# Optimization experiments

Hardware: AMD Instinct MI355X
Metric: run time of the kernel (lower is better)

The kernel has to match this reference:

```python
import jax, jax.numpy as jnp
import numpy as np

B, NA, NB = 2, 2048, 2048
DIM_A, DIM_B = 256, 256
HEADS, DH_A, DH_B = 8, 64, 64
INNER_A, INNER_B = DH_A * HEADS, DH_B * HEADS
EPS = 1e-5


def layer_norm(x, w, b):
    m = jnp.mean(x, axis=-1, keepdims=True)
    v = jnp.mean(jnp.square(x - m), axis=-1, keepdims=True)
    return (x - m) * jax.lax.rsqrt(v + EPS) * w + b


def setup_inputs() -> dict:
    key = jax.random.key(0)
    ks = jax.random.split(key, 16)
    s = 0.02
    return {
        "feat_a": jax.random.normal(ks[0], (B, NA, DIM_A), jnp.float32),
        "feat_b": jax.random.normal(ks[1], (B, NB, DIM_B), jnp.float32),
        "mask_a_b": jax.random.bernoulli(ks[2], 0.5, (B, NA, NB)),
        # linear weights stored (in, out)
        "Wq": jax.random.normal(ks[3], (DIM_A, INNER_B), jnp.float32) * s,
        "bq": jnp.zeros((INNER_B,), jnp.float32),
        "Wk": jax.random.normal(ks[4], (DIM_B, INNER_B), jnp.float32) * s,
        "bk": jnp.zeros((INNER_B,), jnp.float32),
        "Wv": jax.random.normal(ks[5], (DIM_B, INNER_A), jnp.float32) * s,
        "bv": jnp.zeros((INNER_A,), jnp.float32),
        "Wg": jax.random.normal(ks[6], (DIM_A, INNER_A), jnp.float32) * s,
        "bg": jnp.zeros((INNER_A,), jnp.float32),
        "Wo": jax.random.normal(ks[7], (INNER_A, DIM_A), jnp.float32) * s,
        "bo": jnp.zeros((DIM_A,), jnp.float32),
        "ln_a_w": jnp.ones((DIM_A,), jnp.float32),
        "ln_a_b": jnp.zeros((DIM_A,), jnp.float32),
        "ln_b_w": jnp.ones((DIM_B,), jnp.float32),
        "ln_b_b": jnp.zeros((DIM_B,), jnp.float32),
        "qln_w": jnp.ones((INNER_B,), jnp.float32),
        "qln_b": jnp.zeros((INNER_B,), jnp.float32),
        "kln_w": jnp.ones((INNER_B,), jnp.float32),
        "kln_b": jnp.zeros((INNER_B,), jnp.float32),
    }


def reference(feat_a, feat_b, mask_a_b, Wq, bq, Wk, bk, Wv, bv, Wg, bg, Wo, bo,
              ln_a_w, ln_a_b, ln_b_w, ln_b_b, qln_w, qln_b, kln_w, kln_b):
    scale = DH_B ** -0.5
    fa = layer_norm(feat_a, ln_a_w, ln_a_b)            # (b, na, dim_a)
    fb = layer_norm(feat_b, ln_b_w, ln_b_b)            # (b, nb, dim_b)
    q = layer_norm(fa @ Wq + bq, qln_w, qln_b)         # (b, na, inner_b)
    k = layer_norm(fb @ Wk + bk, kln_w, kln_b)         # (b, nb, inner_b)
    v = fb @ Wv + bv                                   # (b, nb, inner_a)
    g = fa @ Wg + bg                                   # (b, na, inner_a)
    q = q.reshape(B, NA, HEADS, DH_B)
    k = k.reshape(B, NB, HEADS, DH_B)
    v = v.reshape(B, NB, HEADS, DH_A)
    g = g.reshape(B, NA, HEADS, DH_A)
    sim = jnp.einsum('bihd,bjhd->bhij', q, k) * scale  # (b, h, na, nb)
    neg = jnp.finfo(sim.dtype).min
    sim = jnp.where(mask_a_b[:, None, :, :], sim, neg)
    attn = jax.nn.softmax(sim, axis=-1)
    out = jnp.einsum('bhij,bjhd->bihd', attn, v)       # (b, na, h, dh_a)
    out = jax.nn.sigmoid(g) * out
    out = out.reshape(B, NA, INNER_A)
    return out @ Wo + bo                               # (b, na, dim_a)
```

## Files before the change

### kernel.cpp

```cpp
#include <hip/hip_runtime.h>
#include <hip/hip_bf16.h>

using bf16 = __hip_bfloat16;
typedef short bf16x8 __attribute__((ext_vector_type(8)));
typedef float f32x4 __attribute__((ext_vector_type(4)));
typedef float f32x16 __attribute__((ext_vector_type(16)));
typedef unsigned short ushort8_t __attribute__((ext_vector_type(8)));
typedef unsigned long long u64;

static constexpr int NA_ = 2048, NB_ = 2048;
static constexpr int H_ = 8, DH_ = 64, INNER_ = 512;
static constexpr int MROWS = 2 * NA_;

#define MFMA32(a, b, c) __builtin_amdgcn_mfma_f32_16x16x32_bf16(a, b, c, 0, 0, 0)
#define MFMA3216(a, b, c) __builtin_amdgcn_mfma_f32_32x32x16_bf16(a, b, c, 0, 0, 0)

__device__ __forceinline__ unsigned short bfbits(float x) {
  bf16 h = __float2bfloat16(x);
  return __builtin_bit_cast(unsigned short, h);
}
__device__ __forceinline__ float b2f(unsigned short u) {
  unsigned v = ((unsigned)u) << 16;
  return __builtin_bit_cast(float, v);
}

__global__ __launch_bounds__(256) void prep_kernel(
    const float* __restrict__ fa_in, const float* __restrict__ fb_in,
    const float* __restrict__ law, const float* __restrict__ lab,
    const float* __restrict__ lbw, const float* __restrict__ lbb,
    bf16* __restrict__ fa, bf16* __restrict__ fb,
    const float* __restrict__ Wq, const float* __restrict__ Wk,
    const float* __restrict__ Wv, const float* __restrict__ Wg,
    const float* __restrict__ Wo,
    bf16* __restrict__ Wqt, bf16* __restrict__ Wkt,
    bf16* __restrict__ Wvt, bf16* __restrict__ Wgt,
    bf16* __restrict__ Woth, bf16* __restrict__ Wotl,
    const void* __restrict__ maskp, u64* __restrict__ mbits) {
  int blk = blockIdx.x;
  int t = threadIdx.x;
  if (blk < 2048) {
    int row = blk * 4 + (t >> 6);
    int lane = t & 63;
    const float *src, *w, *bb;
    bf16* dst;
    int r;
    if (row < MROWS) { src = fa_in; w = law; bb = lab; dst = fa; r = row; }
    else             { src = fb_in; w = lbw; bb = lbb; dst = fb; r = row - MROWS; }
    float4 x = *(const float4*)(src + (size_t)r * 256 + lane * 4);
    float s  = (x.x + x.y) + (x.z + x.w);
    float s2 = (x.x * x.x + x.y * x.y) + (x.z * x.z + x.w * x.w);
#pragma unroll
    for (int m = 32; m >= 1; m >>= 1) { s += __shfl_xor(s, m); s2 += __shfl_xor(s2, m); }
    float mean = s * (1.0f / 256.0f);
    float var  = s2 * (1.0f / 256.0f) - mean * mean;
    float rstd = rsqrtf(var + 1e-5f);
    float4 wv = *(const float4*)(w + lane * 4);
    float4 bv = *(const float4*)(bb + lane * 4);
    ushort4 o;
    o.x = bfbits((x.x - mean) * rstd * wv.x + bv.x);
    o.y = bfbits((x.y - mean) * rstd * wv.y + bv.y);
    o.z = bfbits((x.z - mean) * rstd * wv.z + bv.z);
    o.w = bfbits((x.w - mean) * rstd * wv.w + bv.w);
    *(ushort4*)(dst + (size_t)r * 256 + lane * 4) = o;
  } else if (blk < 4608) {
    int z = (blk - 2048) >> 9;
    int idx = ((blk - 2048) & 511) * 256 + t;
    if (z < 4) {
      const float* W = (z == 0) ? Wq : (z == 1) ? Wk : (z == 2) ? Wv : Wg;
      bf16* Wt = (z == 0) ? Wqt : (z == 1) ? Wkt : (z == 2) ? Wvt : Wgt;
      int kk = idx >> 9, n = idx & 511;
      Wt[n * 256 + kk] = __float2bfloat16(W[idx]);
    } else {
      int kk = idx >> 8, n = idx & 255;
      float w = Wo[idx];
      bf16 hi = __float2bfloat16(w);
      Woth[n * 512 + kk] = hi;
      Wotl[n * 512 + kk] = __float2bfloat16(w - __bfloat162float(hi));
    }
  } else {
    __shared__ unsigned shf[4];
    const unsigned char* mu = (const unsigned char*)maskp;
    bool nz = ((t & 3) != 0) && (mu[t] != 0);
    u64 bal = __ballot(nz);
    if ((t & 63) == 0) shf[t >> 6] = (bal != 0ull) ? 1u : 0u;
    __syncthreads();
    bool m8 = (shf[0] | shf[1] | shf[2] | shf[3]) != 0;
    int lane = t & 63, wid = t >> 6;
    int lb = blk - 4608;
    for (size_t word = (size_t)lb * 4 + wid; word < 131072; word += 8192) {
      size_t e = word * 64 + lane;
      int v = m8 ? (int)mu[e] : ((const int*)maskp)[e];
      u64 b2 = __ballot(v != 0);
      if (lane == 0) mbits[word] = b2;
    }
  }
}

__global__ __launch_bounds__(256) void gemm4_kernel(
    const bf16* __restrict__ fa, const bf16* __restrict__ fb,
    const bf16* __restrict__ Wqt, const bf16* __restrict__ Wkt,
    const bf16* __restrict__ Wgt, const bf16* __restrict__ Wvt,
    const float* __restrict__ bq, const float* __restrict__ bk,
    const float* __restrict__ bg, const float* __restrict__ bv,
    const float* __restrict__ qlw, const float* __restrict__ qlb,
    const float* __restrict__ klw, const float* __restrict__ klb,
    bf16* __restrict__ qo, bf16* __restrict__ ko,
    bf16* __restrict__ gout, bf16* __restrict__ vout) {
  __shared__ __align__(16) char sm[27648];
  int z = blockIdx.z;
  int t = threadIdx.x, wave = t >> 6, lane = t & 63;
  int lm = lane & 15, quad = lane >> 4, q8 = quad * 8;

  if (z < 2) {
    bf16* As = (bf16*)sm;
    float* Pred = (float*)(sm + 16896);
    float* MV   = (float*)(sm + 17408);
    const bf16* A    = z ? fb : fa;
    const bf16* Wt   = z ? Wkt : Wqt;
    const float* bias = z ? bk : bq;
    const float* lw  = z ? klw : qlw;
    const float* lb  = z ? klb : qlb;
    bf16* out        = z ? ko : qo;
    int m0 = blockIdx.x * 16;
#pragma unroll
    for (int i = 0; i < 2; i++) {
      int id = t + 256 * i, r = id >> 5, cg = id & 31;
      *(ushort8_t*)(&As[r * 264 + cg * 8]) =
          *(const ushort8_t*)(A + (size_t)(m0 + r) * 256 + cg * 8);
    }
    __syncthreads();
    int n0w = wave * 128;
    f32x4 acc[8] = {};
    const bf16* wrow[8];
#pragma unroll
    for (int ni = 0; ni < 8; ni++) wrow[ni] = Wt + (size_t)(n0w + ni * 16 + lm) * 256;
#pragma unroll
    for (int ks = 0; ks < 8; ks++) {
      int k0 = ks * 32;
      bf16x8 af = *(const bf16x8*)(&As[lm * 264 + k0 + q8]);
#pragma unroll
      for (int ni = 0; ni < 8; ni++) {
        bf16x8 bf_ = *(const bf16x8*)(wrow[ni] + k0 + q8);
        acc[ni] = MFMA32(af, bf_, acc[ni]);
      }
    }
    float bvv[8];
#pragma unroll
    for (int ni = 0; ni < 8; ni++) bvv[ni] = bias[n0w + ni * 16 + lm];
#pragma unroll
    for (int ni = 0; ni < 8; ni++)
#pragma unroll
      for (int r = 0; r < 4; r++) acc[ni][r] += bvv[ni];
#pragma unroll
    for (int r = 0; r < 4; r++) {
      float s = 0.f, s2 = 0.f;
#pragma unroll
      for (int ni = 0; ni < 8; ni++) { s += acc[ni][r]; s2 += acc[ni][r] * acc[ni][r]; }
#pragma unroll
      for (int m = 1; m <= 8; m <<= 1) { s += __shfl_xor(s, m); s2 += __shfl_xor(s2, m); }
      if (lm == 0) {
        int row = quad * 4 + r;
        Pred[row * 8 + wave * 2]     = s;
        Pred[row * 8 + wave * 2 + 1] = s2;
      }
    }
    __syncthreads();
    if (t < 16) {
      float s = 0.f, s2 = 0.f;
#pragma unroll
      for (int w = 0; w < 4; w++) { s += Pred[t * 8 + w * 2]; s2 += Pred[t * 8 + w * 2 + 1]; }
      float mean = s * (1.0f / 512.0f);
      float var  = s2 * (1.0f / 512.0f) - mean * mean;
      MV[t * 2]     = mean;
      MV[t * 2 + 1] = rsqrtf(var + 1e-5f);
    }
    __syncthreads();
    float lww[8], lbb_[8];
#pragma unroll
    for (int ni = 0; ni < 8; ni++) {
      lww[ni]  = lw[n0w + ni * 16 + lm];
      lbb_[ni] = lb[n0w + ni * 16 + lm];
    }
#pragma unroll
    for (int r = 0; r < 4; r++) {
      int row = quad * 4 + r;
      float mean = MV[row * 2], rstd = MV[row * 2 + 1];
      size_t obase = (size_t)(m0 + row) * 512 + n0w;
#pragma unroll
      for (int ni = 0; ni < 8; ni++)
        out[obase + ni * 16 + lm] =
            __float2bfloat16((acc[ni][r] - mean) * rstd * lww[ni] + lbb_[ni]);
    }
  } else {
    bf16* As = (bf16*)sm;
    bf16* Bs = (bf16*)(sm + 18432);
    const bf16* A    = (z == 3) ? fb : fa;
    const bf16* Wt   = (z == 3) ? Wvt : Wgt;
    const float* bias = (z == 3) ? bv : bg;
    int x = blockIdx.x;
    int m0 = (x >> 3) * 128, n0 = (x & 7) * 64;
    int wm = wave * 32;
    f32x4 acc[2][4] = {};
    for (int k0 = 0; k0 < 256; k0 += 64) {
      __syncthreads();
#pragma unroll
      for (int i = 0; i < 4; i++) {
        int id = t + 256 * i, r = id >> 3, cg = id & 7;
        *(ushort8_t*)(&As[r * 72 + cg * 8]) =
            *(const ushort8_t*)(A + (size_t)(m0 + r) * 256 + k0 + cg * 8);
      }
#pragma unroll
      for (int i = 0; i < 2; i++) {
        int id = t + 256 * i, r = id >> 3, cg = id & 7;
        *(ushort8_t*)(&Bs[r * 72 + cg * 8]) =
            *(const ushort8_t*)(Wt + (size_t)(n0 + r) * 256 + k0 + cg * 8);
      }
      __syncthreads();
#pragma unroll
      for (int kk = 0; kk < 64; kk += 32) {
        bf16x8 af[2], bf_[4];
#pragma unroll
        for (int mi = 0; mi < 2; mi++)
          af[mi] = *(const bf16x8*)(&As[(wm + mi * 16 + lm) * 72 + kk + q8]);
#pragma unroll
        for (int ni = 0; ni < 4; ni++)
          bf_[ni] = *(const bf16x8*)(&Bs[(ni * 16 + lm) * 72 + kk + q8]);
#pragma unroll
        for (int mi = 0; mi < 2; mi++)
#pragma unroll
          for (int ni = 0; ni < 4; ni++)
            acc[mi][ni] = MFMA32(af[mi], bf_[ni], acc[mi][ni]);
      }
    }
    if (z == 2) {
#pragma unroll
      for (int mi = 0; mi < 2; mi++)
#pragma unroll
        for (int ni = 0; ni < 4; ni++) {
          int nn = n0 + ni * 16 + lm;
          float bvv = bias[nn];
          int mb = m0 + wm + mi * 16 + quad * 4;
#pragma unroll
          for (int r = 0; r < 4; r++)
            gout[(size_t)(mb + r) * 512 + nn] = __float2bfloat16(acc[mi][ni][r] + bvv);
        }
    } else {
      __syncthreads();
      bf16* buf = (bf16*)sm;
#pragma unroll
      for (int mi = 0; mi < 2; mi++)
#pragma unroll
        for (int ni = 0; ni < 4; ni++) {
          int d_local = ni * 16 + lm;
          float bvv = bias[n0 + d_local];
          int j_local = wm + mi * 16 + quad * 4;
#pragma unroll
          for (int r = 0; r < 4; r++)
            buf[d_local * 136 + j_local + r] = __float2bfloat16(acc[mi][ni][r] + bvv);
        }
      __syncthreads();
      int bidx2 = m0 >> 11, j0g = m0 & 2047, hh = n0 >> 6;
      int dl = t >> 2, jseg = (t & 3) * 32;
      bf16* dstrow = vout + (size_t)((bidx2 * 8 + hh) * 64 + dl) * 2048 + j0g + jseg;
#pragma unroll
      for (int c = 0; c < 4; c++)
        *(ushort8_t*)(dstrow + c * 8) = *(const ushort8_t*)(&buf[dl * 136 + jseg + c * 8]);
    }
  }
}

__global__ __launch_bounds__(512, 4) void attn_kernel(
    const bf16* __restrict__ q, const bf16* __restrict__ k,
    const bf16* __restrict__ vt, const bf16* __restrict__ g,
    const u64* __restrict__ mbits,
    bf16* __restrict__ gh, bf16* __restrict__ gl) {
  __shared__ __align__(16) char smem[46080];
  bf16* Ks = (bf16*)smem;
  bf16* Vs = (bf16*)(smem + 18432);
  bf16* Qs = (bf16*)(smem + 35840);
  float* Lbuf = (float*)(smem + 45056);
  float* OmA = (float*)smem;
  bf16* Tbuf = (bf16*)(smem + 35840);

  int qt = blockIdx.x, bh = blockIdx.y;
  int bidx = bh >> 3, hh = bh & 7;
  int i0 = qt * 64;
  int t = threadIdx.x, w = t >> 6, lane = t & 63;
  int ig = w & 1, js = w >> 1;
  int l31 = lane & 31, hf = lane >> 5;

  {
    int r = t >> 3, cg = t & 7;
    *(ushort8_t*)(&Qs[r * 72 + cg * 8]) =
        *(const ushort8_t*)(q + (size_t)(bidx * NA_ + i0 + r) * INNER_ + hh * DH_ + cg * 8);
  }
  __syncthreads();
  bf16x8 bq[4];
#pragma unroll
  for (int kt = 0; kt < 4; kt++)
    bq[kt] = *(const bf16x8*)(&Qs[(ig * 32 + l31) * 72 + kt * 16 + hf * 8]);

  f32x16 oT[2];
#pragma unroll
  for (int i = 0; i < 16; i++) { oT[0][i] = 0.f; oT[1][i] = 0.f; }
  float psum = 0.f;
  const float scale2 = 0.125f * 1.44269504088896f;

  const bf16* kb = k + (size_t)(bidx * NB_) * INNER_ + hh * DH_;
  const bf16* vb = vt + (size_t)(bh * DH_) * NB_;
  const u64* mrp = mbits + (size_t)(bidx * NA_ + i0 + ig * 32 + l31) * (NB_ / 64);
  int msh = (js & 1) * 32 + hf * 4;

  for (int it = 0; it < 16; it++) {
    int j0 = it * 128;
    __syncthreads();
#pragma unroll
    for (int i = 0; i < 2; i++) {
      int id = t + 512 * i;
      {
        int r = id >> 3, cg = id & 7;
        *(ushort8_t*)(&Ks[r * 72 + cg * 8]) =
            *(const ushort8_t*)(kb + (size_t)(j0 + r) * INNER_ + cg * 8);
      }
      {
        int d = id >> 4, jg = id & 15;
        *(ushort8_t*)(&Vs[d * 136 + jg * 8]) =
            *(const ushort8_t*)(vb + (size_t)d * NB_ + j0 + jg * 8);
      }
    }
    u64 wm_ = mrp[it * 2 + (js >> 1)];
    __syncthreads();

    f32x16 st;
#pragma unroll
    for (int i = 0; i < 16; i++) st[i] = 0.f;
#pragma unroll
    for (int kt = 0; kt < 4; kt++) {
      bf16x8 ka = *(const bf16x8*)(&Ks[(js * 32 + l31) * 72 + kt * 16 + hf * 8]);
      st = MFMA3216(ka, bq[kt], st);
    }

    unsigned mlo = (unsigned)(wm_ >> msh);
    float pr[16];
#pragma unroll
    for (int reg = 0; reg < 16; reg++) {
      float p = exp2f(st[reg] * scale2);
      unsigned bitpos = (unsigned)((reg & 3) + 8 * (reg >> 2));
      pr[reg] = ((mlo >> bitpos) & 1u) ? p : 0.f;
    }
#pragma unroll
    for (int i = 0; i < 16; i += 4)
      psum += ((pr[i] + pr[i + 1]) + (pr[i + 2] + pr[i + 3]));
    unsigned dw[8];
#pragma unroll
    for (int p = 0; p < 8; p++)
      dw[p] = (unsigned)bfbits(pr[2 * p]) | ((unsigned)bfbits(pr[2 * p + 1]) << 16);

    unsigned rx[8];
#pragma unroll
    for (int p = 0; p < 8; p++) rx[p] = (unsigned)__shfl_xor((int)dw[p], 32);
    unsigned f0[4], f1[4];
    if (hf == 0) {
      f0[0] = dw[0]; f0[1] = dw[1]; f0[2] = rx[0]; f0[3] = rx[1];
      f1[0] = dw[4]; f1[1] = dw[5]; f1[2] = rx[4]; f1[3] = rx[5];
    } else {
      f0[0] = rx[2]; f0[1] = rx[3]; f0[2] = dw[2]; f0[3] = dw[3];
      f1[0] = rx[6]; f1[1] = rx[7]; f1[2] = dw[6]; f1[3] = dw[7];
    }
    bf16x8 pf0 = __builtin_bit_cast(bf16x8, *(uint4*)f0);
    bf16x8 pf1 = __builtin_bit_cast(bf16x8, *(uint4*)f1);

#pragma unroll
    for (int dt = 0; dt < 2; dt++) {
      bf16x8 va0 = *(const bf16x8*)(&Vs[(dt * 32 + l31) * 136 + js * 32 + hf * 8]);
      bf16x8 va1 = *(const bf16x8*)(&Vs[(dt * 32 + l31) * 136 + js * 32 + 16 + hf * 8]);
      oT[dt] = MFMA3216(va0, pf0, oT[dt]);
      oT[dt] = MFMA3216(va1, pf1, oT[dt]);
    }
  }

  psum += __shfl_xor(psum, 32);

  __syncthreads();
  if (lane < 32) Lbuf[js * 64 + ig * 32 + l31] = psum;
  if (js & 1) {
    float* B = OmA + (size_t)(ig * 2 + (js >> 1)) * 2112;
#pragma unroll
    for (int dt = 0; dt < 2; dt++)
#pragma unroll
      for (int reg = 0; reg < 16; reg++) {
        int d = dt * 32 + (reg & 3) + 8 * (reg >> 2) + 4 * hf;
        B[d * 33 + l31] = oT[dt][reg];
      }
  }
  __syncthreads();
  if (!(js & 1)) {
    float* B = OmA + (size_t)(ig * 2 + (js >> 1)) * 2112;
#pragma unroll
    for (int dt = 0; dt < 2; dt++)
#pragma unroll
      for (int reg = 0; reg < 16; reg++) {
        int d = dt * 32 + (reg & 3) + 8 * (reg >> 2) + 4 * hf;
        oT[dt][reg] += B[d * 33 + l31];
      }
  }
  __syncthreads();
  if (js == 2) {
    float* B = OmA + (size_t)(ig * 2 + 1) * 2112;
#pragma unroll
    for (int dt = 0; dt < 2; dt++)
#pragma unroll
      for (int reg = 0; reg < 16; reg++) {
        int d = dt * 32 + (reg & 3) + 8 * (reg >> 2) + 4 * hf;
        B[d * 33 + l31] = oT[dt][reg];
      }
  }
  __syncthreads();
  if (js == 0) {
    float* B = OmA + (size_t)(ig * 2 + 1) * 2112;
#pragma unroll
    for (int dt = 0; dt < 2; dt++)
#pragma unroll
      for (int reg = 0; reg < 16; reg++) {
        int d = dt * 32 + (reg & 3) + 8 * (reg >> 2) + 4 * hf;
        oT[dt][reg] += B[d * 33 + l31];
      }
    int il = ig * 32 + l31;
    float l = ((Lbuf[il] + Lbuf[64 + il]) + (Lbuf[128 + il] + Lbuf[192 + il]));
    float inv = 1.0f / l;
    size_t gpb = (size_t)(bidx * NA_ + i0 + il) * INNER_ + hh * DH_;
#pragma unroll
    for (int dt = 0; dt < 2; dt++)
#pragma unroll
      for (int rg = 0; rg < 4; rg++) {
        int dbase = dt * 32 + rg * 8 + hf * 4;
        short4 g4 = *(const short4*)(g + gpb + dbase);
        unsigned short gu[4] = {(unsigned short)g4.x, (unsigned short)g4.y,
                                (unsigned short)g4.z, (unsigned short)g4.w};
#pragma unroll
        for (int rr = 0; rr < 4; rr++) {
          float gvf = b2f(gu[rr]);
          float sig = 1.0f / (1.0f + __expf(-gvf));
          oT[dt][rg * 4 + rr] = oT[dt][rg * 4 + rr] * inv * sig;
        }
      }
  }
  __syncthreads();
  if (js == 0) {
    int il = ig * 32 + l31;
#pragma unroll
    for (int dt = 0; dt < 2; dt++)
#pragma unroll
      for (int rg = 0; rg < 4; rg++) {
        int dbase = dt * 32 + rg * 8 + hf * 4;
        unsigned w0 = (unsigned)bfbits(oT[dt][rg * 4 + 0]) |
                      ((unsigned)bfbits(oT[dt][rg * 4 + 1]) << 16);
        unsigned w1 = (unsigned)bfbits(oT[dt][rg * 4 + 2]) |
                      ((unsigned)bfbits(oT[dt][rg * 4 + 3]) << 16);
        *(unsigned*)(&Tbuf[il * 72 + dbase])     = w0;
        *(unsigned*)(&Tbuf[il * 72 + dbase + 2]) = w1;
      }
  }
  __syncthreads();
  {
    int ri = t >> 3, seg = t & 7;
    ushort8_t v = *(const ushort8_t*)(&Tbuf[ri * 72 + seg * 8]);
    *(ushort8_t*)(gh + (size_t)(bidx * NA_ + i0 + ri) * INNER_ + hh * DH_ + seg * 8) = v;
  }
  __syncthreads();
  if (js == 0) {
    int il = ig * 32 + l31;
#pragma unroll
    for (int dt = 0; dt < 2; dt++)
#pragma unroll
      for (int rg = 0; rg < 4; rg++) {
        int dbase = dt * 32 + rg * 8 + hf * 4;
        unsigned short lo[4];
#pragma unroll
        for (int rr = 0; rr < 4; rr++) {
          float v = oT[dt][rg * 4 + rr];
          lo[rr] = bfbits(v - b2f(bfbits(v)));
        }
        *(unsigned*)(&Tbuf[il * 72 + dbase])     = (unsigned)lo[0] | ((unsigned)lo[1] << 16);
        *(unsigned*)(&Tbuf[il * 72 + dbase + 2]) = (unsigned)lo[2] | ((unsigned)lo[3] << 16);
      }
  }
  __syncthreads();
  {
    int ri = t >> 3, seg = t & 7;
    ushort8_t v = *(const ushort8_t*)(&Tbuf[ri * 72 + seg * 8]);
    *(ushort8_t*)(gl + (size_t)(bidx * NA_ + i0 + ri) * INNER_ + hh * DH_ + seg * 8) = v;
  }
}

__global__ __launch_bounds__(256) void gemm_split_kernel(
    const bf16* __restrict__ Ah, const bf16* __restrict__ Al,
    const bf16* __restrict__ Bh, const bf16* __restrict__ Bl,
    const float* __restrict__ bias, float* __restrict__ C) {
  constexpr int K = 512, N = 256;
  __shared__ __align__(16) bf16 Ash[32 * 72];
  __shared__ __align__(16) bf16 Asl[32 * 72];
  __shared__ __align__(16) bf16 Bsh[64 * 72];
  __shared__ __align__(16) bf16 Bsl[64 * 72];
  int n0 = blockIdx.x * 64, m0 = blockIdx.y * 32;
  int t = threadIdx.x, wave = t >> 6, lane = t & 63;
  int lm = lane & 15, quad = lane >> 4, q8 = quad * 8;
  int wm = (wave & 1) * 16, wn = (wave >> 1) * 32;
  f32x4 acc[2] = {};
  for (int k0 = 0; k0 < K; k0 += 64) {
    __syncthreads();
    {
      int r = t >> 3, cg = t & 7;
      size_t ga = (size_t)(m0 + r) * K + k0 + cg * 8;
      *(ushort8_t*)(&Ash[r * 72 + cg * 8]) = *(const ushort8_t*)(Ah + ga);
      *(ushort8_t*)(&Asl[r * 72 + cg * 8]) = *(const ushort8_t*)(Al + ga);
    }
#pragma unroll
    for (int i = 0; i < 2; i++) {
      int id = t + 256 * i, r = id >> 3, cg = id & 7;
      size_t gb = (size_t)(n0 + r) * K + k0 + cg * 8;
      *(ushort8_t*)(&Bsh[r * 72 + cg * 8]) = *(const ushort8_t*)(Bh + gb);
      *(ushort8_t*)(&Bsl[r * 72 + cg * 8]) = *(const ushort8_t*)(Bl + gb);
    }
    __syncthreads();
#pragma unroll
    for (int kk = 0; kk < 64; kk += 32) {
      bf16x8 ah = *(const bf16x8*)(&Ash[(wm + lm) * 72 + kk + q8]);
      bf16x8 al = *(const bf16x8*)(&Asl[(wm + lm) * 72 + kk + q8]);
#pragma unroll
      for (int ni = 0; ni < 2; ni++) {
        bf16x8 bh_ = *(const bf16x8*)(&Bsh[(wn + ni * 16 + lm) * 72 + kk + q8]);
        bf16x8 bl_ = *(const bf16x8*)(&Bsl[(wn + ni * 16 + lm) * 72 + kk + q8]);
        acc[ni] = MFMA32(ah, bh_, acc[ni]);
        acc[ni] = MFMA32(ah, bl_, acc[ni]);
        acc[ni] = MFMA32(al, bh_, acc[ni]);
      }
    }
  }
#pragma unroll
  for (int ni = 0; ni < 2; ni++) {
    int n = n0 + wn + ni * 16 + lm;
    float bvv = bias[n];
    int mb = m0 + wm + quad * 4;
#pragma unroll
    for (int r = 0; r < 4; r++) C[(size_t)(mb + r) * N + n] = acc[ni][r] + bvv;
  }
}

extern "C" void kernel_launch(void* const* d_in, const int* in_sizes, int n_in,
                              void* d_out, int out_size, void* d_ws, size_t ws_size,
                              hipStream_t stream) {
  const float* feat_a = (const float*)d_in[0];
  const float* feat_b = (const float*)d_in[1];
  const void*  mask   = d_in[2];
  const float* Wq = (const float*)d_in[3];
  const float* bq = (const float*)d_in[4];
  const float* Wk = (const float*)d_in[5];
  const float* bk = (const float*)d_in[6];
  const float* Wv = (const float*)d_in[7];
  const float* bv = (const float*)d_in[8];
  const float* Wg = (const float*)d_in[9];
  const float* bg = (const float*)d_in[10];
  const float* Wo = (const float*)d_in[11];
  const float* bo = (const float*)d_in[12];
  const float* law = (const float*)d_in[13];
  const float* lab = (const float*)d_in[14];
  const float* lbw = (const float*)d_in[15];
  const float* lbb = (const float*)d_in[16];
  const float* qlw = (const float*)d_in[17];
  const float* qlb = (const float*)d_in[18];
  const float* klw = (const float*)d_in[19];
  const float* klb = (const float*)d_in[20];

  char* ws = (char*)d_ws;
  size_t off = 0;
  auto alloc = [&](size_t bytes) -> void* {
    void* p = ws + off;
    off += (bytes + 255) & ~(size_t)255;
    return p;
  };
  bf16* fa    = (bf16*)alloc((size_t)MROWS * 256 * 2);
  bf16* fb    = (bf16*)alloc((size_t)MROWS * 256 * 2);
  bf16* Wqt   = (bf16*)alloc((size_t)131072 * 2);
  bf16* Wkt   = (bf16*)alloc((size_t)131072 * 2);
  bf16* Wvt   = (bf16*)alloc((size_t)131072 * 2);
  bf16* Wgt   = (bf16*)alloc((size_t)131072 * 2);
  bf16* Woth  = (bf16*)alloc((size_t)131072 * 2);
  bf16* Wotl  = (bf16*)alloc((size_t)131072 * 2);
  bf16* qb_   = (bf16*)alloc((size_t)MROWS * 512 * 2);
  bf16* kb_   = (bf16*)alloc((size_t)MROWS * 512 * 2);
  bf16* vtb   = (bf16*)alloc((size_t)1024 * 2048 * 2);
  bf16* gbuf  = (bf16*)alloc((size_t)MROWS * 512 * 2);
  bf16* gh    = (bf16*)alloc((size_t)MROWS * 512 * 2);
  bf16* gl    = (bf16*)alloc((size_t)MROWS * 512 * 2);
  u64*  mbits = (u64*)alloc((size_t)131072 * 8);

  prep_kernel<<<6656, 256, 0, stream>>>(
      feat_a, feat_b, law, lab, lbw, lbb, fa, fb,
      Wq, Wk, Wv, Wg, Wo, Wqt, Wkt, Wvt, Wgt, Woth, Wotl, mask, mbits);
  gemm4_kernel<<<dim3(256, 1, 4), 256, 0, stream>>>(
      fa, fb, Wqt, Wkt, Wgt, Wvt, bq, bk, bg, bv,
      qlw, qlb, klw, klb, qb_, kb_, gbuf, vtb);
  attn_kernel<<<dim3(32, 16), 512, 0, stream>>>(qb_, kb_, vtb, gbuf, mbits, gh, gl);
  gemm_split_kernel<<<dim3(4, 128), 256, 0, stream>>>(gh, gl, Woth, Wotl, bo, (float*)d_out);
}
```

Baseline: 205.5 us.

## Load K/V directly from global in attention and split query rows across grid

Removes shared-memory staging of K and V tiles in the attention kernel; each wave now loads its own K/V fragments straight from global memory and covers a 32-key slice of a 256-key step. Query rows are split into two 32-row halves via a third grid dimension, which doubles block count and cuts LDS to allow more resident blocks. Partial outputs are reduced serially across 8 waves in shared memory. This removes the per-iteration barriers and LDS traffic but gives up cross-wave reuse of K/V, relying on caches, and issues strided per-lane global loads.

```diff
diff --git a/kernel.cpp b/kernel.cpp
--- a/kernel.cpp
+++ b/kernel.cpp
@@ -269,36 +269,27 @@
   }
 }
 
-__global__ __launch_bounds__(512, 4) void attn_kernel(
+__global__ __launch_bounds__(512, 8) void attn_kernel(
     const bf16* __restrict__ q, const bf16* __restrict__ k,
     const bf16* __restrict__ vt, const bf16* __restrict__ g,
     const u64* __restrict__ mbits,
     bf16* __restrict__ gh, bf16* __restrict__ gl) {
-  __shared__ __align__(16) char smem[46080];
-  bf16* Ks = (bf16*)smem;
-  bf16* Vs = (bf16*)(smem + 18432);
-  bf16* Qs = (bf16*)(smem + 35840);
-  float* Lbuf = (float*)(smem + 45056);
-  float* OmA = (float*)smem;
-  bf16* Tbuf = (bf16*)(smem + 35840);
-
-  int qt = blockIdx.x, bh = blockIdx.y;
+  __shared__ __align__(16) char smem[14336];
+  float* OmB  = (float*)smem;
+  float* Lbuf = (float*)(smem + 8448);
+  bf16*  Tbuf = (bf16*)(smem + 9472);
+
+  int qt = blockIdx.x, bh = blockIdx.y, ig = blockIdx.z;
   int bidx = bh >> 3, hh = bh & 7;
-  int i0 = qt * 64;
-  int t = threadIdx.x, w = t >> 6, lane = t & 63;
-  int ig = w & 1, js = w >> 1;
+  int i0 = qt * 64 + ig * 32;
+  int t = threadIdx.x, js = t >> 6, lane = t & 63;
   int l31 = lane & 31, hf = lane >> 5;
 
-  {
-    int r = t >> 3, cg = t & 7;
-    *(ushort8_t*)(&Qs[r * 72 + cg * 8]) =
-        *(const ushort8_t*)(q + (size_t)(bidx * NA_ + i0 + r) * INNER_ + hh * DH_ + cg * 8);
-  }
-  __syncthreads();
+  const bf16* qrow = q + (size_t)(bidx * NA_ + i0 + l31) * INNER_ + hh * DH_;
   bf16x8 bq[4];
 #pragma unroll
   for (int kt = 0; kt < 4; kt++)
-    bq[kt] = *(const bf16x8*)(&Qs[(ig * 32 + l31) * 72 + kt * 16 + hf * 8]);
+    bq[kt] = *(const bf16x8*)(qrow + kt * 16 + hf * 8);
 
   f32x16 oT[2];
 #pragma unroll
@@ -306,37 +297,22 @@
   float psum = 0.f;
   const float scale2 = 0.125f * 1.44269504088896f;
 
-  const bf16* kb = k + (size_t)(bidx * NB_) * INNER_ + hh * DH_;
-  const bf16* vb = vt + (size_t)(bh * DH_) * NB_;
-  const u64* mrp = mbits + (size_t)(bidx * NA_ + i0 + ig * 32 + l31) * (NB_ / 64);
+  const bf16* klane = k + ((size_t)(bidx * NB_) + js * 32 + l31) * INNER_ + hh * DH_ + hf * 8;
+  const bf16* vlane0 = vt + (size_t)(bh * DH_ + l31) * NB_ + js * 32 + hf * 8;
+  const bf16* vlane1 = vlane0 + (size_t)32 * NB_;
+  const u64* mrp = mbits + (size_t)(bidx * NA_ + i0 + l31) * (NB_ / 64);
   int msh = (js & 1) * 32 + hf * 4;
 
-  for (int it = 0; it < 16; it++) {
-    int j0 = it * 128;
-    __syncthreads();
-#pragma unroll
-    for (int i = 0; i < 2; i++) {
-      int id = t + 512 * i;
-      {
-        int r = id >> 3, cg = id & 7;
-        *(ushort8_t*)(&Ks[r * 72 + cg * 8]) =
-            *(const ushort8_t*)(kb + (size_t)(j0 + r) * INNER_ + cg * 8);
-      }
-      {
-        int d = id >> 4, jg = id & 15;
-        *(ushort8_t*)(&Vs[d * 136 + jg * 8]) =
-            *(const ushort8_t*)(vb + (size_t)d * NB_ + j0 + jg * 8);
-      }
-    }
-    u64 wm_ = mrp[it * 2 + (js >> 1)];
-    __syncthreads();
+  for (int it = 0; it < 8; it++) {
+    size_t j0 = (size_t)it * 256;
+    u64 wm_ = mrp[it * 4 + (js >> 1)];
 
     f32x16 st;
 #pragma unroll
     for (int i = 0; i < 16; i++) st[i] = 0.f;
 #pragma unroll
     for (int kt = 0; kt < 4; kt++) {
-      bf16x8 ka = *(const bf16x8*)(&Ks[(js * 32 + l31) * 72 + kt * 16 + hf * 8]);
+      bf16x8 ka = *(const bf16x8*)(klane + j0 * INNER_ + kt * 16);
       st = MFMA3216(ka, bq[kt], st);
     }
 
@@ -372,63 +348,45 @@
 
 #pragma unroll
     for (int dt = 0; dt < 2; dt++) {
-      bf16x8 va0 = *(const bf16x8*)(&Vs[(dt * 32 + l31) * 136 + js * 32 + hf * 8]);
-      bf16x8 va1 = *(const bf16x8*)(&Vs[(dt * 32 + l31) * 136 + js * 32 + 16 + hf * 8]);
+      const bf16* vl = dt ? vlane1 : vlane0;
+      bf16x8 va0 = *(const bf16x8*)(vl + j0);
+      bf16x8 va1 = *(const bf16x8*)(vl + j0 + 16);
       oT[dt] = MFMA3216(va0, pf0, oT[dt]);
       oT[dt] = MFMA3216(va1, pf1, oT[dt]);
     }
   }
 
   psum += __shfl_xor(psum, 32);
-
-  __syncthreads();
-  if (lane < 32) Lbuf[js * 64 + ig * 32 + l31] = psum;
-  if (js & 1) {
-    float* B = OmA + (size_t)(ig * 2 + (js >> 1)) * 2112;
+  if (lane < 32) Lbuf[js * 32 + l31] = psum;
+
+#pragma unroll 1
+  for (int r = 0; r < 8; r++) {
+    if (js == r) {
+#pragma unroll
+      for (int dt = 0; dt < 2; dt++)
+#pragma unroll
+        for (int reg = 0; reg < 16; reg++) {
+          int d = dt * 32 + (reg & 3) + 8 * (reg >> 2) + 4 * hf;
+          if (r == 0) OmB[d * 33 + l31] = oT[dt][reg];
+          else        OmB[d * 33 + l31] += oT[dt][reg];
+        }
+    }
+    __syncthreads();
+  }
+
+  if (js == 0) {
 #pragma unroll
     for (int dt = 0; dt < 2; dt++)
 #pragma unroll
       for (int reg = 0; reg < 16; reg++) {
         int d = dt * 32 + (reg & 3) + 8 * (reg >> 2) + 4 * hf;
-        B[d * 33 + l31] = oT[dt][reg];
-      }
-  }
-  __syncthreads();
-  if (!(js & 1)) {
-    float* B = OmA + (size_t)(ig * 2 + (js >> 1)) * 2112;
-#pragma unroll
-    for (int dt = 0; dt < 2; dt++)
-#pragma unroll
-      for (int reg = 0; reg < 16; reg++) {
-        int d = dt * 32 + (reg & 3) + 8 * (reg >> 2) + 4 * hf;
-        oT[dt][reg] += B[d * 33 + l31];
-      }
-  }
-  __syncthreads();
-  if (js == 2) {
-    float* B = OmA + (size_t)(ig * 2 + 1) * 2112;
-#pragma unroll
-    for (int dt = 0; dt < 2; dt++)
-#pragma unroll
-      for (int reg = 0; reg < 16; reg++) {
-        int d = dt * 32 + (reg & 3) + 8 * (reg >> 2) + 4 * hf;
-        B[d * 33 + l31] = oT[dt][reg];
-      }
-  }
-  __syncthreads();
-  if (js == 0) {
-    float* B = OmA + (size_t)(ig * 2 + 1) * 2112;
-#pragma unroll
-    for (int dt = 0; dt < 2; dt++)
-#pragma unroll
-      for (int reg = 0; reg < 16; reg++) {
-        int d = dt * 32 + (reg & 3) + 8 * (reg >> 2) + 4 * hf;
-        oT[dt][reg] += B[d * 33 + l31];
-      }
-    int il = ig * 32 + l31;
-    float l = ((Lbuf[il] + Lbuf[64 + il]) + (Lbuf[128 + il] + Lbuf[192 + il]));
+        oT[dt][reg] = OmB[d * 33 + l31];
+      }
+    float l = 0.f;
+#pragma unroll
+    for (int kk = 0; kk < 8; kk++) l += Lbuf[kk * 32 + l31];
     float inv = 1.0f / l;
-    size_t gpb = (size_t)(bidx * NA_ + i0 + il) * INNER_ + hh * DH_;
+    size_t gpb = (size_t)(bidx * NA_ + i0 + l31) * INNER_ + hh * DH_;
 #pragma unroll
     for (int dt = 0; dt < 2; dt++)
 #pragma unroll
@@ -444,10 +402,6 @@
           oT[dt][rg * 4 + rr] = oT[dt][rg * 4 + rr] * inv * sig;
         }
       }
-  }
-  __syncthreads();
-  if (js == 0) {
-    int il = ig * 32 + l31;
 #pragma unroll
     for (int dt = 0; dt < 2; dt++)
 #pragma unroll
@@ -457,19 +411,18 @@
                       ((unsigned)bfbits(oT[dt][rg * 4 + 1]) << 16);
         unsigned w1 = (unsigned)bfbits(oT[dt][rg * 4 + 2]) |
                       ((unsigned)bfbits(oT[dt][rg * 4 + 3]) << 16);
-        *(unsigned*)(&Tbuf[il * 72 + dbase])     = w0;
-        *(unsigned*)(&Tbuf[il * 72 + dbase + 2]) = w1;
+        *(unsigned*)(&Tbuf[l31 * 72 + dbase])     = w0;
+        *(unsigned*)(&Tbuf[l31 * 72 + dbase + 2]) = w1;
       }
   }
   __syncthreads();
-  {
+  if (t < 256) {
     int ri = t >> 3, seg = t & 7;
     ushort8_t v = *(const ushort8_t*)(&Tbuf[ri * 72 + seg * 8]);
     *(ushort8_t*)(gh + (size_t)(bidx * NA_ + i0 + ri) * INNER_ + hh * DH_ + seg * 8) = v;
   }
   __syncthreads();
   if (js == 0) {
-    int il = ig * 32 + l31;
 #pragma unroll
     for (int dt = 0; dt < 2; dt++)
 #pragma unroll
@@ -481,12 +434,12 @@
           float v = oT[dt][rg * 4 + rr];
           lo[rr] = bfbits(v - b2f(bfbits(v)));
         }
-        *(unsigned*)(&Tbuf[il * 72 + dbase])     = (unsigned)lo[0] | ((unsigned)lo[1] << 16);
-        *(unsigned*)(&Tbuf[il * 72 + dbase + 2]) = (unsigned)lo[2] | ((unsigned)lo[3] << 16);
+        *(unsigned*)(&Tbuf[l31 * 72 + dbase])     = (unsigned)lo[0] | ((unsigned)lo[1] << 16);
+        *(unsigned*)(&Tbuf[l31 * 72 + dbase + 2]) = (unsigned)lo[2] | ((unsigned)lo[3] << 16);
       }
   }
   __syncthreads();
-  {
+  if (t < 256) {
     int ri = t >> 3, seg = t & 7;
     ushort8_t v = *(const ushort8_t*)(&Tbuf[ri * 72 + seg * 8]);
     *(ushort8_t*)(gl + (size_t)(bidx * NA_ + i0 + ri) * INNER_ + hh * DH_ + seg * 8) = v;
@@ -601,6 +554,6 @@
   gemm4_kernel<<<dim3(256, 1, 4), 256, 0, stream>>>(
       fa, fb, Wqt, Wkt, Wgt, Wvt, bq, bk, bg, bv,
       qlw, qlb, klw, klb, qb_, kb_, gbuf, vtb);
-  attn_kernel<<<dim3(32, 16), 512, 0, stream>>>(qb_, kb_, vtb, gbuf, mbits, gh, gl);
+  attn_kernel<<<dim3(32, 16, 2), 512, 0, stream>>>(qb_, kb_, vtb, gbuf, mbits, gh, gl);
   gemm_split_kernel<<<dim3(4, 128), 256, 0, stream>>>(gh, gl, Woth, Wotl, bo, (float*)d_out);
 }
```

Measured after the change: 542.9 us. +164.1%, slower.
